# Kernel tuning notes

Hardware: AMD Instinct MI355X
Metric: run time of the kernel (lower is better)

Reference implementation:

```python
import jax, jax.numpy as jnp
import numpy as np

B, N, M, D = 16, 4096, 4096, 3

def setup_inputs() -> dict:
    key = jax.random.key(0)
    k1, k2 = jax.random.split(key)
    x = jax.random.normal(k1, (B, N, D), dtype=jnp.float32)
    y = jax.random.normal(k2, (B, M, D), dtype=jnp.float32)
    return {"x": x, "y": y}

def reference(x, y):
    # pairwise L2 distance matrix C: [B, N, M]
    diff = x[:, :, None, :] - y[:, None, :, :]          # [B, N, M, D]
    C = jnp.sqrt(jnp.sum(diff * diff, axis=-1))          # [B, N, M]
    d1 = jnp.min(C, axis=-1).mean(axis=-1)               # x -> nearest y, mean over N: [B]
    d2 = jnp.min(C, axis=-2).mean(axis=-1)               # y -> nearest x, mean over M: [B]
    cost = (d1 + d2) / 2.0                               # reduction='none'
    return cost
```

## Files before the change

### kernel.cpp

```cpp
#include <hip/hip_runtime.h>
#include <cstdint>
#include <cstddef>

#define S      4096
#define BATCH  16
#define BLK    256
#define YSPAN  1024
#define CHUNK  256
#define NTILE  (CHUNK / 32)
#define NCHUNK (YSPAN / CHUNK)
#define ROWS_PER_BLOCK 128
#define XC_N   (S / ROWS_PER_BLOCK)
#define YC_N   (S / YSPAN)

typedef _Float16 half8   __attribute__((ext_vector_type(8)));
typedef float    floatx16 __attribute__((ext_vector_type(16)));

__device__ inline unsigned pack2(_Float16 lo, _Float16 hi) {
    unsigned short a = __builtin_bit_cast(unsigned short, lo);
    unsigned short b = __builtin_bit_cast(unsigned short, hi);
    return (unsigned)a | ((unsigned)b << 16);
}

__global__ __launch_bounds__(BLK, 3) void chamfer_mfma_kernel(
    const float* __restrict__ x, const float* __restrict__ y,
    float* __restrict__ ws0, float* __restrict__ ws1,
    float* __restrict__ out)
{
    const int b    = blockIdx.y;
    const int xc   = blockIdx.x;
    const int yc   = blockIdx.z;
    const int tid  = threadIdx.x;
    const int lane = tid & 63;
    const int wave = tid >> 6;
    const int hi32 = lane >> 5;
    const int l31  = lane & 31;

    if (xc == 0 && yc == 0 && tid == 0) out[b] = 0.0f;

    __shared__ uint4 ldsb[2][NTILE][64];
    __shared__ float colmin2[4][YSPAN];

    for (int i = tid; i < 2 * NTILE * 32; i += BLK) {
        int bu = i / (NTILE * 32); int r = i % (NTILE * 32);
        ldsb[bu][r >> 5][32 + (r & 31)].z = 0x00003C00u;
        ldsb[bu][r >> 5][32 + (r & 31)].w = 0u;
    }

    const int row = xc * ROWS_PER_BLOCK + wave * 32 + l31;
    const float* xp = x + ((size_t)b * S + row) * 3;
    const float x0 = xp[0], x1 = xp[1], x2 = xp[2];
    const float xn = 0.5f * (x0 * x0 + x1 * x1 + x2 * x2);
    const _Float16 xh0 = (_Float16)x0, xh1 = (_Float16)x1, xh2 = (_Float16)x2;
    const _Float16 xl0 = (_Float16)(x0 - (float)xh0);
    const _Float16 xl1 = (_Float16)(x1 - (float)xh1);
    const _Float16 xl2 = (_Float16)(x2 - (float)xh2);
    const _Float16 xnh = (_Float16)xn;
    const _Float16 xnl = (_Float16)(xn - (float)xnh);
    half8 afrag;
    if (hi32 == 0) {
        afrag[0] = -xh0; afrag[1] = -xh1; afrag[2] = -xh2;
        afrag[3] = -xh0; afrag[4] = -xh1; afrag[5] = -xh2;
        afrag[6] = -xl0; afrag[7] = -xl1;
    } else {
        afrag[0] = -xl2; afrag[1] = (_Float16)1.0f; afrag[2] = (_Float16)1.0f;
        afrag[3] = xnh;  afrag[4] = xnl;
        afrag[5] = (_Float16)0.0f; afrag[6] = (_Float16)0.0f; afrag[7] = (_Float16)0.0f;
    }

    floatx16 runrow;
#pragma unroll
    for (int r = 0; r < 16; ++r) runrow[r] = 3.0e38f;
    const floatx16 zeroacc = {};

    const int ybase = yc * YSPAN;
    const float* ysrc = y + ((size_t)b * S + ybase) * 3;

    auto stage = [&](int cc) {
        const int buf = cc & 1;
        const int p   = cc * CHUNK + tid;
        const float* yp = ysrc + (size_t)p * 3;
        const float y0 = yp[0], y1 = yp[1], y2 = yp[2];
        const float h  = 0.5f * (y0 * y0 + y1 * y1 + y2 * y2);
        const _Float16 a0 = (_Float16)y0, a1 = (_Float16)y1, a2 = (_Float16)y2;
        const _Float16 b0 = (_Float16)(y0 - (float)a0);
        const _Float16 b1 = (_Float16)(y1 - (float)a1);
        const _Float16 b2 = (_Float16)(y2 - (float)a2);
        const _Float16 hh = (_Float16)h;
        const _Float16 hl = (_Float16)(h - (float)hh);
        const int t = tid >> 5, col = tid & 31;
        ldsb[buf][t][col] = make_uint4(pack2(a0, a1), pack2(a2, b0),
                                       pack2(b1, b2), pack2(a0, a1));
        *(uint2*)&ldsb[buf][t][32 + col] =
            make_uint2(pack2(a2, hh), pack2(hl, (_Float16)1.0f));
    };

    stage(0);
    __syncthreads();

#pragma unroll 1
    for (int c = 0; c < NCHUNK; ++c) {
        if (c + 1 < NCHUNK) stage(c + 1);
        const int buf = c & 1;
        float mc[NTILE];
#pragma unroll
        for (int t = 0; t < NTILE; ++t) {
            const uint4 braw = ldsb[buf][t][lane];
            const half8 bfrag = __builtin_bit_cast(half8, braw);
            const floatx16 d =
                __builtin_amdgcn_mfma_f32_32x32x16_f16(afrag, bfrag, zeroacc, 0, 0, 0);
#pragma unroll
            for (int r = 0; r < 16; ++r) runrow[r] = fminf(runrow[r], d[r]);
            const float m1 = fminf(fminf(d[0],  d[1]),  d[2]);
            const float m2 = fminf(fminf(d[3],  d[4]),  d[5]);
            const float m3 = fminf(fminf(d[6],  d[7]),  d[8]);
            const float m4 = fminf(fminf(d[9],  d[10]), d[11]);
            const float m5 = fminf(fminf(d[12], d[13]), d[14]);
            const float m6 = fminf(fminf(m1, m2), m3);
            const float m7 = fminf(fminf(m4, m5), d[15]);
            mc[t] = fminf(m6, m7);
        }
#pragma unroll
        for (int t = 0; t < NTILE; ++t) {
            const float v = fminf(mc[t], __shfl_xor(mc[t], 32));
            if (hi32 == 0) colmin2[wave][c * CHUNK + t * 32 + l31] = v;
        }
        __syncthreads();
    }

#pragma unroll
    for (int r = 0; r < 16; ++r) {
        float v = runrow[r];
        v = fminf(v, __shfl_xor(v, 1));
        v = fminf(v, __shfl_xor(v, 2));
        v = fminf(v, __shfl_xor(v, 4));
        v = fminf(v, __shfl_xor(v, 8));
        v = fminf(v, __shfl_xor(v, 16));
        runrow[r] = v;
    }
    if (l31 == 0) {
        float* w0 = ws0 + ((size_t)yc * BATCH + b) * S
                        + xc * ROWS_PER_BLOCK + wave * 32;
#pragma unroll
        for (int r = 0; r < 16; ++r) {
            const int rr = (r & 3) + 8 * (r >> 2) + 4 * hi32;
            w0[rr] = runrow[r];
        }
    }

    __syncthreads();

    float* w1 = ws1 + ((size_t)xc * BATCH + b) * S + ybase;
    for (int i = tid; i < YSPAN; i += BLK) {
        const float m = fminf(fminf(colmin2[0][i], colmin2[1][i]),
                              fminf(colmin2[2][i], colmin2[3][i]));
        w1[i] = m;
    }
}

#define RSEG   (S / BLK)
__global__ __launch_bounds__(BLK) void chamfer_reduce_kernel(
    const float* __restrict__ ws0, const float* __restrict__ ws1,
    float* __restrict__ out)
{
    const int b   = blockIdx.y;
    const int i   = blockIdx.x * BLK + threadIdx.x;
    const int tid = threadIdx.x;

    float mx = 3.0e38f;
#pragma unroll
    for (int yc = 0; yc < YC_N; ++yc)
        mx = fminf(mx, ws0[((size_t)yc * BATCH + b) * S + i]);
    float my = 3.0e38f;
#pragma unroll
    for (int xc = 0; xc < XC_N; ++xc)
        my = fminf(my, ws1[((size_t)xc * BATCH + b) * S + i]);

    float s = sqrtf(2.0f * fmaxf(mx, 0.0f)) + sqrtf(2.0f * fmaxf(my, 0.0f));

    __shared__ float red[BLK];
    red[tid] = s;
    __syncthreads();
    for (int off = BLK / 2; off > 0; off >>= 1) {
        if (tid < off) red[tid] += red[tid + off];
        __syncthreads();
    }
    if (tid == 0) atomicAdd(&out[b], red[0] * (0.5f / (float)S));
}

#define P   8
#define FMC 1024
#define OUTER_PER_BLK (BLK * P)
__global__ __launch_bounds__(BLK) void chamfer_full_kernel(
    const float* __restrict__ x, const float* __restrict__ y,
    float* __restrict__ out)
{
    const int role = blockIdx.z;
    const int b    = blockIdx.y;
    const int oc   = blockIdx.x;
    const float* __restrict__ outer = (role == 0) ? x : y;
    const float* __restrict__ inner = (role == 0) ? y : x;
    const int tid = threadIdx.x;
    const int n0  = oc * OUTER_PER_BLK;

    __shared__ float4 lds[FMC];

    float nx0[P], nx1[P], nx2[P], xn[P], tmin[P];
#pragma unroll
    for (int p = 0; p < P; ++p) {
        const int n = n0 + p * BLK + tid;
        const float* xp = outer + ((size_t)b * S + n) * 3;
        const float a0 = xp[0], a1 = xp[1], a2 = xp[2];
        nx0[p] = -a0; nx1[p] = -a1; nx2[p] = -a2;
        xn[p]  = a0 * a0 + a1 * a1 + a2 * a2;
        tmin[p] = 3.0e38f;
    }

    for (int m0 = 0; m0 < S; m0 += FMC) {
        __syncthreads();
        for (int i = tid; i < FMC; i += BLK) {
            const float* yp = inner + ((size_t)b * S + m0 + i) * 3;
            const float a0 = yp[0], a1 = yp[1], a2 = yp[2];
            lds[i] = make_float4(a0, a1, a2,
                                 0.5f * (a0 * a0 + a1 * a1 + a2 * a2));
        }
        __syncthreads();
#pragma unroll 4
        for (int j = 0; j < FMC; ++j) {
            const float4 v = lds[j];
#pragma unroll
            for (int p = 0; p < P; ++p) {
                const float t = fmaf(nx0[p], v.x,
                                 fmaf(nx1[p], v.y,
                                  fmaf(nx2[p], v.z, v.w)));
                tmin[p] = fminf(tmin[p], t);
            }
        }
    }

    float s = 0.0f;
#pragma unroll
    for (int p = 0; p < P; ++p)
        s += sqrtf(fmaxf(fmaf(2.0f, tmin[p], xn[p]), 0.0f));

    __shared__ float red[BLK];
    red[tid] = s;
    __syncthreads();
    for (int off = BLK / 2; off > 0; off >>= 1) {
        if (tid < off) red[tid] += red[tid + off];
        __syncthreads();
    }
    if (tid == 0) atomicAdd(&out[b], red[0] * (0.5f / (float)S));
}

extern "C" void kernel_launch(void* const* d_in, const int* in_sizes, int n_in,
                              void* d_out, int out_size, void* d_ws, size_t ws_size,
                              hipStream_t stream) {
    const float* x = (const float*)d_in[0];
    const float* y = (const float*)d_in[1];
    float* out = (float*)d_out;

    const size_t n_ws0 = (size_t)YC_N * BATCH * S;
    const size_t n_ws1 = (size_t)XC_N * BATCH * S;
    const size_t need  = (n_ws0 + n_ws1) * sizeof(float);
    if (ws_size >= need) {
        float* ws0 = (float*)d_ws;
        float* ws1 = ws0 + n_ws0;
        chamfer_mfma_kernel<<<dim3(XC_N, BATCH, YC_N), BLK, 0, stream>>>(
            x, y, ws0, ws1, out);
        chamfer_reduce_kernel<<<dim3(RSEG, BATCH), BLK, 0, stream>>>(
            ws0, ws1, out);
    } else {
        hipMemsetAsync(d_out, 0, BATCH * sizeof(float), stream);
        chamfer_full_kernel<<<dim3(S / OUTER_PER_BLK, BATCH, 2), BLK, 0, stream>>>(
            x, y, out);
    }
}
```

Baseline: 41.28 us.

## Compute both directions as row-min passes instead of extracting column minima

Each block now takes a role (x-vs-y or y-vs-x) and computes only row minima via MFMA, so the column-min reduction, cross-lane shuffles and LDS column buffer are dropped. The workspace for the reverse direction shrinks from per-x-chunk to per-slab, so the reduce kernel reads less. In exchange the MFMA distance computations double. Launch bounds are raised to target higher occupancy, which may add register pressure.

New measurement: 38.89 us. 1.06x faster.

```diff
diff --git a/kernel.cpp b/kernel.cpp
--- a/kernel.cpp
+++ b/kernel.cpp
@@ -22,24 +22,28 @@
     return (unsigned)a | ((unsigned)b << 16);
 }
 
-__global__ __launch_bounds__(BLK, 3) void chamfer_mfma_kernel(
+__global__ __launch_bounds__(BLK, 6) void chamfer_mfma_kernel(
     const float* __restrict__ x, const float* __restrict__ y,
     float* __restrict__ ws0, float* __restrict__ ws1,
     float* __restrict__ out)
 {
     const int b    = blockIdx.y;
     const int xc   = blockIdx.x;
-    const int yc   = blockIdx.z;
+    const int role = blockIdx.z >> 2;
+    const int slab = blockIdx.z & 3;
     const int tid  = threadIdx.x;
     const int lane = tid & 63;
     const int wave = tid >> 6;
     const int hi32 = lane >> 5;
     const int l31  = lane & 31;
 
-    if (xc == 0 && yc == 0 && tid == 0) out[b] = 0.0f;
+    const float* __restrict__ outer = role ? y : x;
+    const float* __restrict__ inner = role ? x : y;
+    float* __restrict__ ws = role ? ws1 : ws0;
+
+    if (xc == 0 && blockIdx.z == 0 && tid == 0) out[b] = 0.0f;
 
     __shared__ uint4 ldsb[2][NTILE][64];
-    __shared__ float colmin2[4][YSPAN];
 
     for (int i = tid; i < 2 * NTILE * 32; i += BLK) {
         int bu = i / (NTILE * 32); int r = i % (NTILE * 32);
@@ -48,23 +52,23 @@
     }
 
     const int row = xc * ROWS_PER_BLOCK + wave * 32 + l31;
-    const float* xp = x + ((size_t)b * S + row) * 3;
-    const float x0 = xp[0], x1 = xp[1], x2 = xp[2];
-    const float xn = 0.5f * (x0 * x0 + x1 * x1 + x2 * x2);
-    const _Float16 xh0 = (_Float16)x0, xh1 = (_Float16)x1, xh2 = (_Float16)x2;
-    const _Float16 xl0 = (_Float16)(x0 - (float)xh0);
-    const _Float16 xl1 = (_Float16)(x1 - (float)xh1);
-    const _Float16 xl2 = (_Float16)(x2 - (float)xh2);
-    const _Float16 xnh = (_Float16)xn;
-    const _Float16 xnl = (_Float16)(xn - (float)xnh);
+    const float* op = outer + ((size_t)b * S + row) * 3;
+    const float o0 = op[0], o1 = op[1], o2 = op[2];
+    const float on = 0.5f * (o0 * o0 + o1 * o1 + o2 * o2);
+    const _Float16 oh0 = (_Float16)o0, oh1 = (_Float16)o1, oh2 = (_Float16)o2;
+    const _Float16 ol0 = (_Float16)(o0 - (float)oh0);
+    const _Float16 ol1 = (_Float16)(o1 - (float)oh1);
+    const _Float16 ol2 = (_Float16)(o2 - (float)oh2);
+    const _Float16 onh = (_Float16)on;
+    const _Float16 onl = (_Float16)(on - (float)onh);
     half8 afrag;
     if (hi32 == 0) {
-        afrag[0] = -xh0; afrag[1] = -xh1; afrag[2] = -xh2;
-        afrag[3] = -xh0; afrag[4] = -xh1; afrag[5] = -xh2;
-        afrag[6] = -xl0; afrag[7] = -xl1;
+        afrag[0] = -oh0; afrag[1] = -oh1; afrag[2] = -oh2;
+        afrag[3] = -oh0; afrag[4] = -oh1; afrag[5] = -oh2;
+        afrag[6] = -ol0; afrag[7] = -ol1;
     } else {
-        afrag[0] = -xl2; afrag[1] = (_Float16)1.0f; afrag[2] = (_Float16)1.0f;
-        afrag[3] = xnh;  afrag[4] = xnl;
+        afrag[0] = -ol2; afrag[1] = (_Float16)1.0f; afrag[2] = (_Float16)1.0f;
+        afrag[3] = onh;  afrag[4] = onl;
         afrag[5] = (_Float16)0.0f; afrag[6] = (_Float16)0.0f; afrag[7] = (_Float16)0.0f;
     }
 
@@ -73,19 +77,19 @@
     for (int r = 0; r < 16; ++r) runrow[r] = 3.0e38f;
     const floatx16 zeroacc = {};
 
-    const int ybase = yc * YSPAN;
-    const float* ysrc = y + ((size_t)b * S + ybase) * 3;
+    const int ibase = slab * YSPAN;
+    const float* isrc = inner + ((size_t)b * S + ibase) * 3;
 
     auto stage = [&](int cc) {
         const int buf = cc & 1;
         const int p   = cc * CHUNK + tid;
-        const float* yp = ysrc + (size_t)p * 3;
-        const float y0 = yp[0], y1 = yp[1], y2 = yp[2];
-        const float h  = 0.5f * (y0 * y0 + y1 * y1 + y2 * y2);
-        const _Float16 a0 = (_Float16)y0, a1 = (_Float16)y1, a2 = (_Float16)y2;
-        const _Float16 b0 = (_Float16)(y0 - (float)a0);
-        const _Float16 b1 = (_Float16)(y1 - (float)a1);
-        const _Float16 b2 = (_Float16)(y2 - (float)a2);
+        const float* ip = isrc + (size_t)p * 3;
+        const float i0 = ip[0], i1 = ip[1], i2 = ip[2];
+        const float h  = 0.5f * (i0 * i0 + i1 * i1 + i2 * i2);
+        const _Float16 a0 = (_Float16)i0, a1 = (_Float16)i1, a2 = (_Float16)i2;
+        const _Float16 b0 = (_Float16)(i0 - (float)a0);
+        const _Float16 b1 = (_Float16)(i1 - (float)a1);
+        const _Float16 b2 = (_Float16)(i2 - (float)a2);
         const _Float16 hh = (_Float16)h;
         const _Float16 hl = (_Float16)(h - (float)hh);
         const int t = tid >> 5, col = tid & 31;
@@ -102,7 +106,6 @@
     for (int c = 0; c < NCHUNK; ++c) {
         if (c + 1 < NCHUNK) stage(c + 1);
         const int buf = c & 1;
-        float mc[NTILE];
 #pragma unroll
         for (int t = 0; t < NTILE; ++t) {
             const uint4 braw = ldsb[buf][t][lane];
@@ -111,19 +114,6 @@
                 __builtin_amdgcn_mfma_f32_32x32x16_f16(afrag, bfrag, zeroacc, 0, 0, 0);
 #pragma unroll
             for (int r = 0; r < 16; ++r) runrow[r] = fminf(runrow[r], d[r]);
-            const float m1 = fminf(fminf(d[0],  d[1]),  d[2]);
-            const float m2 = fminf(fminf(d[3],  d[4]),  d[5]);
-            const float m3 = fminf(fminf(d[6],  d[7]),  d[8]);
-            const float m4 = fminf(fminf(d[9],  d[10]), d[11]);
-            const float m5 = fminf(fminf(d[12], d[13]), d[14]);
-            const float m6 = fminf(fminf(m1, m2), m3);
-            const float m7 = fminf(fminf(m4, m5), d[15]);
-            mc[t] = fminf(m6, m7);
-        }
-#pragma unroll
-        for (int t = 0; t < NTILE; ++t) {
-            const float v = fminf(mc[t], __shfl_xor(mc[t], 32));
-            if (hi32 == 0) colmin2[wave][c * CHUNK + t * 32 + l31] = v;
         }
         __syncthreads();
     }
@@ -139,22 +129,13 @@
         runrow[r] = v;
     }
     if (l31 == 0) {
-        float* w0 = ws0 + ((size_t)yc * BATCH + b) * S
-                        + xc * ROWS_PER_BLOCK + wave * 32;
+        float* w = ws + ((size_t)slab * BATCH + b) * S
+                      + xc * ROWS_PER_BLOCK + wave * 32;
 #pragma unroll
         for (int r = 0; r < 16; ++r) {
             const int rr = (r & 3) + 8 * (r >> 2) + 4 * hi32;
-            w0[rr] = runrow[r];
-        }
-    }
-
-    __syncthreads();
-
-    float* w1 = ws1 + ((size_t)xc * BATCH + b) * S + ybase;
-    for (int i = tid; i < YSPAN; i += BLK) {
-        const float m = fminf(fminf(colmin2[0][i], colmin2[1][i]),
-                              fminf(colmin2[2][i], colmin2[3][i]));
-        w1[i] = m;
+            w[rr] = runrow[r];
+        }
     }
 }
 
@@ -167,14 +148,12 @@
     const int i   = blockIdx.x * BLK + threadIdx.x;
     const int tid = threadIdx.x;
 
-    float mx = 3.0e38f;
-#pragma unroll
-    for (int yc = 0; yc < YC_N; ++yc)
-        mx = fminf(mx, ws0[((size_t)yc * BATCH + b) * S + i]);
-    float my = 3.0e38f;
-#pragma unroll
-    for (int xc = 0; xc < XC_N; ++xc)
-        my = fminf(my, ws1[((size_t)xc * BATCH + b) * S + i]);
+    float mx = 3.0e38f, my = 3.0e38f;
+#pragma unroll
+    for (int sl = 0; sl < YC_N; ++sl) {
+        mx = fminf(mx, ws0[((size_t)sl * BATCH + b) * S + i]);
+        my = fminf(my, ws1[((size_t)sl * BATCH + b) * S + i]);
+    }
 
     float s = sqrtf(2.0f * fmaxf(mx, 0.0f)) + sqrtf(2.0f * fmaxf(my, 0.0f));
 
@@ -260,13 +239,12 @@
     const float* y = (const float*)d_in[1];
     float* out = (float*)d_out;
 
-    const size_t n_ws0 = (size_t)YC_N * BATCH * S;
-    const size_t n_ws1 = (size_t)XC_N * BATCH * S;
-    const size_t need  = (n_ws0 + n_ws1) * sizeof(float);
+    const size_t n_ws = (size_t)YC_N * BATCH * S;
+    const size_t need = 2 * n_ws * sizeof(float);
     if (ws_size >= need) {
         float* ws0 = (float*)d_ws;
-        float* ws1 = ws0 + n_ws0;
-        chamfer_mfma_kernel<<<dim3(XC_N, BATCH, YC_N), BLK, 0, stream>>>(
+        float* ws1 = ws0 + n_ws;
+        chamfer_mfma_kernel<<<dim3(XC_N, BATCH, 2 * YC_N), BLK, 0, stream>>>(
             x, y, ws0, ws1, out);
         chamfer_reduce_kernel<<<dim3(RSEG, BATCH), BLK, 0, stream>>>(
             ws0, ws1, out);
```
